# Kernel tuning notes

Hardware: AMD Instinct MI355X
Metric: run time of the kernel (lower is better)

## Reference

```python
import jax, jax.numpy as jnp
import numpy as np

N_HEAD = 16
D_HEAD = 64
D_MODEL = 1024
SCALE = 1.0 / D_HEAD ** 0.5


def setup_inputs() -> dict:
    key = jax.random.key(0)
    k1, k2 = jax.random.split(key)
    h = jax.random.normal(k1, (2048, 2, D_MODEL), dtype=jnp.float32)
    # torch Linear weight layout: [out_features, in_features]
    w_qkv = jax.random.normal(k2, (3 * N_HEAD * D_HEAD, D_MODEL), dtype=jnp.float32) * (D_MODEL ** -0.5)
    return {"h": h, "w_qkv": w_qkv}


def reference(h, w_qkv):
    qlen, bsz, _ = h.shape
    heads = h @ w_qkv.T  # [qlen, bsz, 3*n_head*d_head]
    head_q, head_k, head_v = jnp.split(heads, 3, axis=-1)
    head_q = head_q.reshape(qlen, bsz, N_HEAD, D_HEAD)
    head_k = head_k.reshape(qlen, bsz, N_HEAD, D_HEAD)
    head_v = head_v.reshape(qlen, bsz, N_HEAD, D_HEAD)
    attn_score = jnp.einsum('ibnd,jbnd->ijbn', head_q, head_k) * SCALE
    attn_prob = jax.nn.softmax(attn_score, axis=1)  # softmax over key dim j
    # dropout is identity at p=0.0 / eval mode
    attn_vec = jnp.einsum('ijbn,jbnd->ibnd', attn_prob, head_v)
    attn_vec = attn_vec.reshape(qlen, bsz, N_HEAD * D_HEAD)
    return attn_vec, attn_prob
```

## Files before the change

### kernel.cpp

```cpp
#include <hip/hip_runtime.h>

typedef _Float16 f16;
typedef f16 f16x8 __attribute__((ext_vector_type(8)));
typedef f16 f16x4 __attribute__((ext_vector_type(4)));
typedef float f32x4 __attribute__((ext_vector_type(4)));

#define QLEN 2048
#define BSZ 2
#define NH 16
#define DH 64
#define DM 1024
#define NBN (BSZ*NH)
#define SCALE 0.125f

static __device__ __forceinline__ f32x4 mfma16(f16x8 a, f16x8 b, f32x4 c) {
  return __builtin_amdgcn_mfma_f32_16x16x32_f16(a, b, c, 0, 0, 0);
}

static __device__ __forceinline__ void gload_lds16(const void* g, void* l) {
  __builtin_amdgcn_global_load_lds((const __attribute__((address_space(1))) unsigned int*)g,
                                   (__attribute__((address_space(3))) unsigned int*)l,
                                   16, 0, 0);
}

static __device__ __forceinline__ void barrier_lds() {
  __builtin_amdgcn_sched_barrier(0);
  asm volatile("s_waitcnt lgkmcnt(0)" ::: "memory");
  __builtin_amdgcn_s_barrier();
  __builtin_amdgcn_sched_barrier(0);
}

__global__ __launch_bounds__(256) void cvt_f32_f16(const float* __restrict__ s,
                                                   f16* __restrict__ d, int n4) {
  int idx = blockIdx.x * 256 + threadIdx.x;
  if (idx >= n4) return;
  f32x4 v = ((const f32x4*)s)[idx];
  f16x4 o;
#pragma unroll
  for (int q = 0; q < 4; ++q) o[q] = (f16)v[q];
  ((f16x4*)d)[idx] = o;
}

__global__ __launch_bounds__(256) void qkv_gemm(const f16* __restrict__ A, const f16* __restrict__ W,
                                                f16* __restrict__ Qs, f16* __restrict__ Ks,
                                                f16* __restrict__ Vt) {
  __shared__ f16 As[128 * 32];
  __shared__ f16 Bs[128 * 32];
  const int bid = blockIdx.x;
  const int r0 = (bid & 31) << 7;
  const int c0 = (bid >> 5) << 7;
  const int t = threadIdx.x;
  const int lane = t & 63, w = t >> 6;
  const int wr = (w >> 1) << 6, wc = (w & 1) << 6;
  const int l15 = lane & 15, lhi = lane >> 4;

  f32x4 acc[4][4] = {};

  const f16* ga = A + (size_t)(r0 + (t >> 2)) * DM + ((t & 3) << 3);
  const f16* gb = W + (size_t)(c0 + (t >> 2)) * DM + ((t & 3) << 3);
  char* la = (char*)As + w * 1024;
  char* lb = (char*)Bs + w * 1024;

  for (int k0 = 0; k0 < DM; k0 += 32) {
    __syncthreads();
    gload_lds16(ga + k0, la);
    gload_lds16(ga + k0 + (size_t)64 * DM, la + 4096);
    gload_lds16(gb + k0, lb);
    gload_lds16(gb + k0 + (size_t)64 * DM, lb + 4096);
    __syncthreads();
    f16x8 af[4], bf[4];
#pragma unroll
    for (int m = 0; m < 4; ++m)
      af[m] = *(const f16x8*)&As[(wr + m * 16 + l15) * 32 + lhi * 8];
#pragma unroll
    for (int n = 0; n < 4; ++n)
      bf[n] = *(const f16x8*)&Bs[(wc + n * 16 + l15) * 32 + lhi * 8];
#pragma unroll
    for (int m = 0; m < 4; ++m)
#pragma unroll
      for (int n = 0; n < 4; ++n)
        acc[m][n] = mfma16(af[m], bf[n], acc[m][n]);
  }

  const int part = c0 >> 10;
#pragma unroll
  for (int m = 0; m < 4; ++m) {
#pragma unroll
    for (int n = 0; n < 4; ++n) {
#pragma unroll
      for (int q = 0; q < 4; ++q) {
        int r = r0 + wr + m * 16 + lhi * 4 + q;
        int c = c0 + wc + n * 16 + l15;
        int i = r >> 1, b = r & 1;
        int nh = (c >> 6) & 15, d = c & 63;
        int bn = b * 16 + nh;
        f16 v = (f16)acc[m][n][q];
        if (part == 0)       Qs[((size_t)bn * QLEN + i) * DH + d] = v;
        else if (part == 1)  Ks[((size_t)bn * QLEN + i) * DH + d] = v;
        else                 Vt[((size_t)bn * DH + d) * QLEN + i] = v;
      }
    }
  }
}

__global__ __launch_bounds__(256) void flash_attn(const f16* __restrict__ Qs, const f16* __restrict__ Ks,
                                                  const f16* __restrict__ Vt, float* __restrict__ av,
                                                  float* __restrict__ sm, float* __restrict__ srl) {
  __shared__ f16 plds[4][16 * 32];
  const int bid = blockIdx.x;
  const int bn = bid >> 4, ib = bid & 15;
  const int t = threadIdx.x, lane = t & 63, w = t >> 6;
  const int l15 = lane & 15, lhi = lane >> 4;
  const int i0 = (ib << 7) + (w << 5);
  const f16* Qb = Qs + ((size_t)bn << 17);
  const f16* Kb = Ks + ((size_t)bn << 17);
  const f16* Vb = Vt + ((size_t)bn << 17);
  f16* pw = plds[w];

  f16x8 qf[2][2];
#pragma unroll
  for (int rg = 0; rg < 2; ++rg)
#pragma unroll
    for (int kc = 0; kc < 2; ++kc)
      qf[rg][kc] = *(const f16x8*)&Qb[(size_t)(i0 + rg * 16 + l15) * DH + kc * 32 + lhi * 8];

  f32x4 o[2][4] = {};
  float mrun[2][4], lrun[2][4];
#pragma unroll
  for (int rg = 0; rg < 2; ++rg)
#pragma unroll
    for (int q = 0; q < 4; ++q) { mrun[rg][q] = -1e30f; lrun[rg][q] = 0.f; }

  for (int j0 = 0; j0 < QLEN; j0 += 32) {
    f16x8 kf[2][2], vf[4];
#pragma unroll
    for (int jc = 0; jc < 2; ++jc)
#pragma unroll
      for (int kc = 0; kc < 2; ++kc)
        kf[jc][kc] = *(const f16x8*)&Kb[(size_t)(j0 + jc * 16 + l15) * DH + kc * 32 + lhi * 8];
#pragma unroll
    for (int dc = 0; dc < 4; ++dc)
      vf[dc] = *(const f16x8*)&Vb[(size_t)(dc * 16 + l15) * QLEN + j0 + lhi * 8];

#pragma unroll
    for (int rg = 0; rg < 2; ++rg) {
      f32x4 s[2];
#pragma unroll
      for (int jc = 0; jc < 2; ++jc) {
        f32x4 z = {0.f, 0.f, 0.f, 0.f};
        z = mfma16(qf[rg][0], kf[jc][0], z);
        z = mfma16(qf[rg][1], kf[jc][1], z);
        s[jc] = z;
      }
      float p[2][4], alpha[4];
#pragma unroll
      for (int q = 0; q < 4; ++q) {
        float v0 = s[0][q] * SCALE, v1 = s[1][q] * SCALE;
        float tm = fmaxf(v0, v1);
        tm = fmaxf(tm, __shfl_xor(tm, 1));
        tm = fmaxf(tm, __shfl_xor(tm, 2));
        tm = fmaxf(tm, __shfl_xor(tm, 4));
        tm = fmaxf(tm, __shfl_xor(tm, 8));
        float mnew = fmaxf(mrun[rg][q], tm);
        alpha[q] = __expf(mrun[rg][q] - mnew);
        mrun[rg][q] = mnew;
        p[0][q] = __expf(v0 - mnew);
        p[1][q] = __expf(v1 - mnew);
        float r = p[0][q] + p[1][q];
        r += __shfl_xor(r, 1);
        r += __shfl_xor(r, 2);
        r += __shfl_xor(r, 4);
        r += __shfl_xor(r, 8);
        lrun[rg][q] = lrun[rg][q] * alpha[q] + r;
      }
#pragma unroll
      for (int dc = 0; dc < 4; ++dc)
#pragma unroll
        for (int q = 0; q < 4; ++q)
          o[rg][dc][q] *= alpha[q];
#pragma unroll
      for (int jc = 0; jc < 2; ++jc)
#pragma unroll
        for (int q = 0; q < 4; ++q)
          pw[(lhi * 4 + q) * 32 + jc * 16 + l15] = (f16)p[jc][q];
      f16x8 pa = *(const f16x8*)&pw[l15 * 32 + lhi * 8];
#pragma unroll
      for (int dc = 0; dc < 4; ++dc)
        o[rg][dc] = mfma16(pa, vf[dc], o[rg][dc]);
    }
  }

  const int b = bn >> 4, nh = bn & 15;
#pragma unroll
  for (int rg = 0; rg < 2; ++rg)
#pragma unroll
    for (int dc = 0; dc < 4; ++dc)
#pragma unroll
      for (int q = 0; q < 4; ++q) {
        int i = i0 + rg * 16 + lhi * 4 + q;
        av[((size_t)i * BSZ + b) * (NH * DH) + nh * DH + dc * 16 + l15] =
            o[rg][dc][q] / lrun[rg][q];
      }
  if (l15 == 0) {
#pragma unroll
    for (int rg = 0; rg < 2; ++rg)
#pragma unroll
      for (int q = 0; q < 4; ++q) {
        int i = i0 + rg * 16 + lhi * 4 + q;
        sm[bn * QLEN + i] = mrun[rg][q];
        srl[bn * QLEN + i] = 1.0f / lrun[rg][q];
      }
  }
}

#define LOADK(buf, chn)                                                        \
  do {                                                                         \
    _Pragma("unroll") for (int bl_ = 0; bl_ < 4; ++bl_) {                      \
      const f16* Kb_ = Ks + (((size_t)(w4 + bl_)) << 17) +                     \
                       (size_t)(j0 + (chn) * 16 + l15) * DH + lhi * 8;         \
      buf[bl_][0] = *(const f16x8*)(Kb_);                                      \
      buf[bl_][1] = *(const f16x8*)(Kb_ + 32);                                 \
    }                                                                          \
  } while (0)

#define CHUNK(cur, nxt, ch)                                                    \
  do {                                                                         \
    const int jbase_ = j0 + (ch) * 16;                                         \
    f16 stv[4][4];                                                             \
    _Pragma("unroll") for (int bl_ = 0; bl_ < 4; ++bl_) {                      \
      f32x4 z = {0.f, 0.f, 0.f, 0.f};                                          \
      z = mfma16(qf[bl_][0], cur[bl_][0], z);                                  \
      z = mfma16(qf[bl_][1], cur[bl_][1], z);                                  \
      _Pragma("unroll") for (int q_ = 0; q_ < 4; ++q_)                         \
        stv[bl_][q_] = (f16)(__expf(z[q_] * SCALE - mm[bl_][q_]) * rl[bl_][q_]); \
    }                                                                          \
    __builtin_amdgcn_sched_barrier(0);                                         \
    { const int nch_ = ((ch) + 1 < 16) ? (ch) + 1 : 15; LOADK(nxt, nch_); }    \
    __builtin_amdgcn_sched_barrier(0);                                         \
    f16* tb_ = tile[(ch) & 1];                                                 \
    _Pragma("unroll") for (int q_ = 0; q_ < 4; ++q_) {                         \
      const int i_l = lhi * 4 + q_;                                            \
      const int jl = l15;                                                      \
      f16x4 v = {stv[0][q_], stv[1][q_], stv[2][q_], stv[3][q_]};              \
      *(f16x4*)&tb_[(i_l * 16 + jl) * 32 + ((w ^ (jl & 7)) << 2)] = v;         \
    }                                                                          \
    barrier_lds();                                                             \
    _Pragma("unroll") for (int p_ = 0; p_ < 2; ++p_) {                         \
      const int i_l = p_ * 8 + w;                                              \
      f16x8 v = *(const f16x8*)&tb_[(i_l * 16 + jl_s) * 32 + (quad << 3)];     \
      f16x4 vl = {v[0], v[1], v[2], v[3]};                                     \
      f16x4 vh = {v[4], v[5], v[6], v[7]};                                     \
      f16x4 fa = hsw ? vh : vl;                                                \
      f16x4 fb = hsw ? vl : vh;                                                \
      f32x4 lo = {(float)fa[0], (float)fa[1], (float)fa[2], (float)fa[3]};     \
      f32x4 hi = {(float)fb[0], (float)fb[1], (float)fb[2], (float)fb[3]};     \
      float* op = pout + ((size_t)(i0 + i_l) * QLEN + jbase_ + jl_s) * NBN + o * 8; \
      *(f32x4*)op = lo;                                                        \
      *(f32x4*)(op + 4) = hi;                                                  \
    }                                                                          \
  } while (0)

__global__ __launch_bounds__(512, 1) void write_probs(const f16* __restrict__ Qs, const f16* __restrict__ Ks,
                                                      const float* __restrict__ sm, const float* __restrict__ srl,
                                                      float* __restrict__ pout) {
  __shared__ f16 tile[2][16 * 16 * 32];
  const int bid = blockIdx.x;
  const int it = bid >> 3, jt = bid & 7;
  const int i0 = it << 4, j0 = jt << 8;
  const int t = threadIdx.x, lane = t & 63, w = t >> 6;
  const int l15 = lane & 15, lhi = lane >> 4;
  const int w4 = w * 4;

  f16x8 qf[4][2];
  float mm[4][4], rl[4][4];
#pragma unroll
  for (int bl = 0; bl < 4; ++bl) {
    const int bn = w4 + bl;
    const f16* Qb = Qs + ((size_t)bn << 17);
#pragma unroll
    for (int kc = 0; kc < 2; ++kc)
      qf[bl][kc] = *(const f16x8*)&Qb[(size_t)(i0 + l15) * DH + kc * 32 + lhi * 8];
#pragma unroll
    for (int q = 0; q < 4; ++q) {
      const int i = i0 + lhi * 4 + q;
      mm[bl][q] = sm[bn * QLEN + i];
      rl[bl][q] = srl[bn * QLEN + i];
    }
  }

  const int o = t & 3;
  const int jl_s = (t >> 2) & 15;
  const int quad = o ^ ((jl_s & 7) >> 1);
  const bool hsw = (jl_s & 1);

  f16x8 kfA[4][2], kfB[4][2];
  LOADK(kfA, 0);

  for (int ch = 0; ch < 16; ch += 2) {
    CHUNK(kfA, kfB, ch);
    CHUNK(kfB, kfA, ch + 1);
  }
}

extern "C" void kernel_launch(void* const* d_in, const int* in_sizes, int n_in,
                              void* d_out, int out_size, void* d_ws, size_t ws_size,
                              hipStream_t stream) {
  const float* h  = (const float*)d_in[0];
  const float* wq = (const float*)d_in[1];
  float* av   = (float*)d_out;
  float* pout = av + (size_t)QLEN * BSZ * NH * DH;

  char* ws = (char*)d_ws;
  f16* hh  = (f16*)ws;
  f16* wh  = (f16*)(ws + (8u << 20));
  f16* Qsc = (f16*)(ws + (16u << 20));
  f16* Ksc = (f16*)(ws + (24u << 20));
  f16* Vtc = (f16*)(ws + (32u << 20));
  float* smv  = (float*)(ws + (40u << 20));
  float* srlv = (float*)(ws + (40u << 20) + (QLEN * NBN * 4));

  const int nh4 = QLEN * BSZ * DM / 4;
  const int nw4 = 3 * NH * DH * DM / 4;
  cvt_f32_f16<<<nh4 / 256, 256, 0, stream>>>(h, hh, nh4);
  cvt_f32_f16<<<nw4 / 256, 256, 0, stream>>>(wq, wh, nw4);
  qkv_gemm<<<32 * 24, 256, 0, stream>>>(hh, wh, Qsc, Ksc, Vtc);
  flash_attn<<<NBN * 16, 256, 0, stream>>>(Qsc, Ksc, Vtc, av, smv, srlv);
  write_probs<<<128 * 8, 512, 0, stream>>>(Qsc, Ksc, smv, srlv, pout);
}
```

Baseline: 373.4 us.

## Batch four key chunks per LDS phase before writing probabilities

The probability-writing kernel now stages four 16-key subchunks into one larger LDS tile and only then synchronizes and streams the tile out to global memory. Before, each 16-key chunk was double-buffered and needed its own barrier. This cuts barrier count per block and changes the store pattern to 16 rows of 64 keys with a new swizzle. The cost is a larger shared-memory tile, an extra barrier per phase to protect reuse, and less overlap between compute and stores inside a phase.

```diff
diff --git a/kernel.cpp b/kernel.cpp
--- a/kernel.cpp
+++ b/kernel.cpp
@@ -223,9 +223,8 @@
     }                                                                          \
   } while (0)
 
-#define CHUNK(cur, nxt, ch)                                                    \
+#define SUBCHUNK(cur, nxt, ch, sub)                                            \
   do {                                                                         \
-    const int jbase_ = j0 + (ch) * 16;                                         \
     f16 stv[4][4];                                                             \
     _Pragma("unroll") for (int bl_ = 0; bl_ < 4; ++bl_) {                      \
       f32x4 z = {0.f, 0.f, 0.f, 0.f};                                          \
@@ -237,33 +236,18 @@
     __builtin_amdgcn_sched_barrier(0);                                         \
     { const int nch_ = ((ch) + 1 < 16) ? (ch) + 1 : 15; LOADK(nxt, nch_); }    \
     __builtin_amdgcn_sched_barrier(0);                                         \
-    f16* tb_ = tile[(ch) & 1];                                                 \
     _Pragma("unroll") for (int q_ = 0; q_ < 4; ++q_) {                         \
       const int i_l = lhi * 4 + q_;                                            \
-      const int jl = l15;                                                      \
+      const int jl = (sub) * 16 + l15;                                         \
       f16x4 v = {stv[0][q_], stv[1][q_], stv[2][q_], stv[3][q_]};              \
-      *(f16x4*)&tb_[(i_l * 16 + jl) * 32 + ((w ^ (jl & 7)) << 2)] = v;         \
-    }                                                                          \
-    barrier_lds();                                                             \
-    _Pragma("unroll") for (int p_ = 0; p_ < 2; ++p_) {                         \
-      const int i_l = p_ * 8 + w;                                              \
-      f16x8 v = *(const f16x8*)&tb_[(i_l * 16 + jl_s) * 32 + (quad << 3)];     \
-      f16x4 vl = {v[0], v[1], v[2], v[3]};                                     \
-      f16x4 vh = {v[4], v[5], v[6], v[7]};                                     \
-      f16x4 fa = hsw ? vh : vl;                                                \
-      f16x4 fb = hsw ? vl : vh;                                                \
-      f32x4 lo = {(float)fa[0], (float)fa[1], (float)fa[2], (float)fa[3]};     \
-      f32x4 hi = {(float)fb[0], (float)fb[1], (float)fb[2], (float)fb[3]};     \
-      float* op = pout + ((size_t)(i0 + i_l) * QLEN + jbase_ + jl_s) * NBN + o * 8; \
-      *(f32x4*)op = lo;                                                        \
-      *(f32x4*)(op + 4) = hi;                                                  \
+      *(f16x4*)&tile[(i_l * 64 + jl) * 32 + ((w ^ (l15 & 7)) << 2)] = v;       \
     }                                                                          \
   } while (0)
 
 __global__ __launch_bounds__(512, 1) void write_probs(const f16* __restrict__ Qs, const f16* __restrict__ Ks,
                                                       const float* __restrict__ sm, const float* __restrict__ srl,
                                                       float* __restrict__ pout) {
-  __shared__ f16 tile[2][16 * 16 * 32];
+  __shared__ f16 tile[16 * 64 * 32];
   const int bid = blockIdx.x;
   const int it = bid >> 3, jt = bid & 7;
   const int i0 = it << 4, j0 = jt << 8;
@@ -288,17 +272,28 @@
     }
   }
 
-  const int o = t & 3;
-  const int jl_s = (t >> 2) & 15;
-  const int quad = o ^ ((jl_s & 7) >> 1);
-  const bool hsw = (jl_s & 1);
+  const int j_s = t >> 3;
+  const int o = t & 7;
+  const int swz = o ^ (j_s & 7);
 
   f16x8 kfA[4][2], kfB[4][2];
   LOADK(kfA, 0);
 
-  for (int ch = 0; ch < 16; ch += 2) {
-    CHUNK(kfA, kfB, ch);
-    CHUNK(kfB, kfA, ch + 1);
+  for (int ph = 0; ph < 4; ++ph) {
+    const int c0 = ph * 4;
+    SUBCHUNK(kfA, kfB, c0 + 0, 0);
+    SUBCHUNK(kfB, kfA, c0 + 1, 1);
+    SUBCHUNK(kfA, kfB, c0 + 2, 2);
+    SUBCHUNK(kfB, kfA, c0 + 3, 3);
+    barrier_lds();
+#pragma unroll
+    for (int r = 0; r < 16; ++r) {
+      f16x4 v = *(const f16x4*)&tile[(r * 64 + j_s) * 32 + (swz << 2)];
+      f32x4 ov = {(float)v[0], (float)v[1], (float)v[2], (float)v[3]};
+      float* op = pout + ((size_t)(i0 + r) * QLEN + j0 + ph * 64 + j_s) * NBN + o * 4;
+      *(f32x4*)op = ov;
+    }
+    barrier_lds();
   }
 }
 
```

After: 360.7 us. 3.4% less time.
